# Kernel optimization log

Hardware: AMD Instinct MI355X
Metric: run time of the kernel (lower is better)

The kernel has to match this reference:

```python
import jax, jax.numpy as jnp
import numpy as np

B, H = 8192, 768


def _mk_linear(key, fan_in, fan_out):
    k1, k2 = jax.random.split(key)
    lim = 1.0 / np.sqrt(fan_in)
    W = jax.random.uniform(k1, (fan_out, fan_in), jnp.float32, -lim, lim)
    b = jax.random.uniform(k2, (fan_out,), jnp.float32, -lim, lim)
    return W, b


def setup_inputs() -> dict:
    key = jax.random.key(0)
    ks = jax.random.split(key, 6)
    modal_a = jax.random.normal(ks[0], (B, H), jnp.float32)
    modal_b = jax.random.normal(ks[1], (B, H), jnp.float32)
    W1m, b1m = _mk_linear(ks[2], H, H)
    W2m, b2m = _mk_linear(ks[3], H, H)
    W1v, b1v = _mk_linear(ks[4], H, H)
    W2v, b2v = _mk_linear(ks[5], H, H)
    return {"modal_a": modal_a, "modal_b": modal_b,
            "W1m": W1m, "b1m": b1m, "W2m": W2m, "b2m": b2m,
            "W1v": W1v, "b1v": b1v, "W2v": W2v, "b2v": b2v}


def reference(modal_a, modal_b, W1m, b1m, W2m, b2m, W1v, b1v, W2v, b2v):
    # mlp_mu: Linear -> Tanh -> Linear
    mu = jnp.tanh(modal_a @ W1m.T + b1m) @ W2m.T + b2m              # [B,H]
    # mlp_logvar: Linear -> Tanh -> Linear -> Tanh
    logvar = jnp.tanh(jnp.tanh(modal_a @ W1v.T + b1v) @ W2v.T + b2v)  # [B,H]
    inv_var = jnp.exp(-logvar)

    positive = -(mu - modal_b) ** 2 * 0.5 * inv_var                  # [B,H]

    # mean_j (mu[j] - mu[i])^2 = E[mu^2] - 2*mu[i]*E[mu] + mu[i]^2  (per feature dim)
    # Algebraic reduction of the O(B^2*H) tile in the original code.
    mu_mean = jnp.mean(mu, axis=0)                                   # [H]
    mu_sq_mean = jnp.mean(mu * mu, axis=0)                           # [H]
    pair_sq = mu_sq_mean - 2.0 * mu * mu_mean + mu * mu              # [B,H]
    negative = -pair_sq * 0.5 * inv_var                              # [B,H]

    pos_sum = jnp.sum(positive, axis=-1)                             # [B]
    neg_sum = jnp.sum(negative, axis=-1)                             # [B]
    lld = jnp.mean(pos_sum)
    bound = jnp.mean(pos_sum - neg_sum)
    return (lld, bound)
```

## Files before the change

kernel.cpp:

```cpp
#include <hip/hip_runtime.h>
#include <math.h>

typedef float v4f __attribute__((ext_vector_type(4)));
typedef short bf16x8 __attribute__((ext_vector_type(8)));

#define AS1 __attribute__((address_space(1)))
#define AS3 __attribute__((address_space(3)))

static constexpr int Bn = 8192;
static constexpr int Hn = 768;
static constexpr float invB = 1.0f / 8192.0f;

__device__ __forceinline__ short f32_to_bf16(float x) {
    union { float f; unsigned u; } v; v.f = x;
    unsigned r = (v.u + 0x7FFFu + ((v.u >> 16) & 1u)) >> 16;
    return (short)r;
}

__device__ __forceinline__ float fast_tanh(float x) {
    float xc = fminf(fmaxf(x, -15.0f), 15.0f);
    float e = __expf(2.0f * xc);
    float r = __builtin_amdgcn_rcpf(e + 1.0f);
    return 1.0f - 2.0f * r;
}

__global__ void prep_kernel(const float* __restrict__ A,
                            const float* __restrict__ W1m, const float* __restrict__ W2m,
                            const float* __restrict__ W1v, const float* __restrict__ W2v,
                            short* __restrict__ A_bf,
                            short* __restrict__ W1m_bf, short* __restrict__ W2m_bf,
                            short* __restrict__ W1v_bf, short* __restrict__ W2v_bf,
                            float* __restrict__ zbuf, int nzero) {
    const int tid = blockIdx.x * blockDim.x + threadIdx.x;
    if (tid < nzero) zbuf[tid] = 0.0f;
    constexpr int A4 = Bn * Hn / 4;
    constexpr int W4 = Hn * Hn / 4;
    const int total = A4 + 4 * W4;
    const int stride = gridDim.x * blockDim.x;
    for (int i = tid; i < total; i += stride) {
        const float* s; short* d; int j;
        if (i < A4) { s = A; d = A_bf; j = i; }
        else {
            int k = i - A4; int w = k / W4; j = k - w * W4;
            s = (w == 0) ? W1m : (w == 1) ? W2m : (w == 2) ? W1v : W2v;
            d = (w == 0) ? W1m_bf : (w == 1) ? W2m_bf : (w == 2) ? W1v_bf : W2v_bf;
        }
        float4 v = ((const float4*)s)[j];
        short4 o;
        o.x = f32_to_bf16(v.x); o.y = f32_to_bf16(v.y);
        o.z = f32_to_bf16(v.z); o.w = f32_to_bf16(v.w);
        ((short4*)d)[j] = o;
    }
}

__launch_bounds__(256, 3)
__global__ void gemm_l1(const short* __restrict__ A_g,
                        const short* __restrict__ Wm_g, const short* __restrict__ Wv_g,
                        const float* __restrict__ bm, const float* __restrict__ bv,
                        short* __restrict__ outm, short* __restrict__ outv) {
    constexpr int K = Hn;
    __shared__ __align__(16) short smem[16384];
    short* As = smem;
    short* Ws = smem + 8192;

    const int z = blockIdx.z;
    const short* W = z ? Wv_g : Wm_g;
    const float* bias = z ? bv : bm;
    short* out = z ? outv : outm;

    const int t = threadIdx.x;
    const int row0 = blockIdx.x * 128;
    const int col0 = blockIdx.y * 128;
    const int w = t >> 6, lane = t & 63;
    const int wm = w >> 1, wn = w & 1;
    const int lr = lane & 15, quad = lane >> 4;

    const int rt = t >> 3;
    const int bsrc = (t & 7) ^ (rt & 7);

    const short* pA[4]; const short* pW[4];
#pragma unroll
    for (int i = 0; i < 4; ++i) {
        pA[i] = A_g + (size_t)(row0 + i * 32 + rt) * K + bsrc * 8;
        pW[i] = W + (size_t)(col0 + i * 32 + rt) * K + bsrc * 8;
    }

    v4f acc[4][4] = {};

    for (int k0 = 0; k0 < K; k0 += 64) {
#pragma unroll
        for (int i = 0; i < 4; ++i) {
            __builtin_amdgcn_global_load_lds((AS1 void*)pA[i], (AS3 void*)&As[i * 2048 + t * 8], 16, 0, 0);
            __builtin_amdgcn_global_load_lds((AS1 void*)pW[i], (AS3 void*)&Ws[i * 2048 + t * 8], 16, 0, 0);
            pA[i] += 64; pW[i] += 64;
        }
        __syncthreads();
#pragma unroll
        for (int s = 0; s < 2; ++s) {
            const int kb = s * 4 + quad;
            bf16x8 af[4], bfr[4];
#pragma unroll
            for (int mt = 0; mt < 4; ++mt) {
                int m = wm * 64 + mt * 16 + lr;
                af[mt] = *(const bf16x8*)&As[m * 64 + ((kb ^ (m & 7)) << 3)];
            }
#pragma unroll
            for (int nt = 0; nt < 4; ++nt) {
                int n = wn * 64 + nt * 16 + lr;
                bfr[nt] = *(const bf16x8*)&Ws[n * 64 + ((kb ^ (n & 7)) << 3)];
            }
#pragma unroll
            for (int mt = 0; mt < 4; ++mt)
#pragma unroll
                for (int nt = 0; nt < 4; ++nt)
                    acc[mt][nt] = __builtin_amdgcn_mfma_f32_16x16x32_bf16(af[mt], bfr[nt], acc[mt][nt], 0, 0, 0);
        }
        __syncthreads();
    }

#pragma unroll
    for (int nt = 0; nt < 4; ++nt) {
        const int col_l = wn * 64 + nt * 16 + lr;
        const float bc = bias[col0 + col_l];
#pragma unroll
        for (int mt = 0; mt < 4; ++mt) {
#pragma unroll
            for (int r = 0; r < 4; ++r) {
                const int row_l = wm * 64 + mt * 16 + quad * 4 + r;
                smem[row_l * 128 + col_l] = f32_to_bf16(fast_tanh(acc[mt][nt][r] + bc));
            }
        }
    }
    __syncthreads();
#pragma unroll
    for (int p = 0; p < 8; ++p) {
        const int row_l = p * 16 + (t >> 4);
        const int seg = (t & 15) * 8;
        bf16x8 v = *(const bf16x8*)&smem[row_l * 128 + seg];
        *(bf16x8*)&out[(size_t)(row0 + row_l) * Hn + col0 + seg] = v;
    }
}

__launch_bounds__(256, 3)
__global__ void gemm_l2(const short* __restrict__ Am_g, const short* __restrict__ Av_g,
                        const short* __restrict__ Wm_g, const short* __restrict__ Wv_g,
                        const float* __restrict__ bm, const float* __restrict__ bv,
                        const float* __restrict__ mb,
                        float* __restrict__ cs, float* __restrict__ cs2,
                        float* __restrict__ siv, float* __restrict__ sivmu,
                        float* __restrict__ accum, float* __restrict__ outp) {
    constexpr int K = Hn;
    __shared__ __align__(16) short As_m[128 * 64];
    __shared__ __align__(16) short As_v[128 * 64];
    __shared__ __align__(16) short Ws_m[64 * 64];
    __shared__ __align__(16) short Ws_v[64 * 64];

    const int t = threadIdx.x;
    const int row0 = blockIdx.x * 128;
    const int col0 = blockIdx.y * 64;
    const int w = t >> 6, lane = t & 63;
    const int wm = w >> 1, wn = w & 1;
    const int lr = lane & 15, quad = lane >> 4;

    const int rt = t >> 3;
    const int bsrc = (t & 7) ^ (rt & 7);

    const short* pAm[4]; const short* pAv[4]; const short* pWm[2]; const short* pWv[2];
#pragma unroll
    for (int i = 0; i < 4; ++i) {
        pAm[i] = Am_g + (size_t)(row0 + i * 32 + rt) * K + bsrc * 8;
        pAv[i] = Av_g + (size_t)(row0 + i * 32 + rt) * K + bsrc * 8;
    }
#pragma unroll
    for (int i = 0; i < 2; ++i) {
        pWm[i] = Wm_g + (size_t)(col0 + i * 32 + rt) * K + bsrc * 8;
        pWv[i] = Wv_g + (size_t)(col0 + i * 32 + rt) * K + bsrc * 8;
    }

    v4f accm[4][2] = {}, accv[4][2] = {};

    for (int k0 = 0; k0 < K; k0 += 64) {
#pragma unroll
        for (int i = 0; i < 4; ++i) {
            __builtin_amdgcn_global_load_lds((AS1 void*)pAm[i], (AS3 void*)&As_m[i * 2048 + t * 8], 16, 0, 0);
            __builtin_amdgcn_global_load_lds((AS1 void*)pAv[i], (AS3 void*)&As_v[i * 2048 + t * 8], 16, 0, 0);
            pAm[i] += 64; pAv[i] += 64;
        }
#pragma unroll
        for (int i = 0; i < 2; ++i) {
            __builtin_amdgcn_global_load_lds((AS1 void*)pWm[i], (AS3 void*)&Ws_m[i * 2048 + t * 8], 16, 0, 0);
            __builtin_amdgcn_global_load_lds((AS1 void*)pWv[i], (AS3 void*)&Ws_v[i * 2048 + t * 8], 16, 0, 0);
            pWm[i] += 64; pWv[i] += 64;
        }
        __syncthreads();
#pragma unroll
        for (int s = 0; s < 2; ++s) {
            const int kb = s * 4 + quad;
            bf16x8 am[4], av[4], bmf[2], bvf[2];
#pragma unroll
            for (int mt = 0; mt < 4; ++mt) {
                int m = wm * 64 + mt * 16 + lr;
                int off = m * 64 + ((kb ^ (m & 7)) << 3);
                am[mt] = *(const bf16x8*)&As_m[off];
                av[mt] = *(const bf16x8*)&As_v[off];
            }
#pragma unroll
            for (int nt = 0; nt < 2; ++nt) {
                int n = wn * 32 + nt * 16 + lr;
                int off = n * 64 + ((kb ^ (n & 7)) << 3);
                bmf[nt] = *(const bf16x8*)&Ws_m[off];
                bvf[nt] = *(const bf16x8*)&Ws_v[off];
            }
#pragma unroll
            for (int mt = 0; mt < 4; ++mt)
#pragma unroll
                for (int nt = 0; nt < 2; ++nt) {
                    accm[mt][nt] = __builtin_amdgcn_mfma_f32_16x16x32_bf16(am[mt], bmf[nt], accm[mt][nt], 0, 0, 0);
                    accv[mt][nt] = __builtin_amdgcn_mfma_f32_16x16x32_bf16(av[mt], bvf[nt], accv[mt][nt], 0, 0, 0);
                }
        }
        __syncthreads();
    }

    float pos = 0.f, q = 0.f;
#pragma unroll
    for (int nt = 0; nt < 2; ++nt) {
        const int col = col0 + wn * 32 + nt * 16 + lr;
        const float bmc = bm[col], bvc = bv[col];
        float c1 = 0.f, c2 = 0.f, c3 = 0.f, c4 = 0.f;
#pragma unroll
        for (int mt = 0; mt < 4; ++mt) {
#pragma unroll
            for (int r = 0; r < 4; ++r) {
                const int row = row0 + wm * 64 + mt * 16 + quad * 4 + r;
                float mu = accm[mt][nt][r] + bmc;
                float tv = fast_tanh(accv[mt][nt][r] + bvc);
                float iv = __expf(-tv);
                float mbv = mb[(size_t)row * Hn + col];
                float d = mu - mbv;
                pos += iv * d * d;
                q   += iv * mu * mu;
                c1 += mu; c2 += mu * mu; c3 += iv; c4 += iv * mu;
            }
        }
        c1 += __shfl_xor(c1, 16); c1 += __shfl_xor(c1, 32);
        c2 += __shfl_xor(c2, 16); c2 += __shfl_xor(c2, 32);
        c3 += __shfl_xor(c3, 16); c3 += __shfl_xor(c3, 32);
        c4 += __shfl_xor(c4, 16); c4 += __shfl_xor(c4, 32);
        if (quad == 0) {
            atomicAdd(&cs[col], c1);
            atomicAdd(&cs2[col], c2);
            atomicAdd(&siv[col], c3);
            atomicAdd(&sivmu[col], c4);
        }
    }
    for (int off = 32; off > 0; off >>= 1) {
        pos += __shfl_down(pos, off);
        q   += __shfl_down(q, off);
    }
    __shared__ float redP[4], redQ[4];
    if (lane == 0) { redP[w] = pos; redQ[w] = q; }
    __syncthreads();
    __shared__ int is_last;
    if (t == 0) {
        atomicAdd(&accum[0], redP[0] + redP[1] + redP[2] + redP[3]);
        atomicAdd(&accum[1], redQ[0] + redQ[1] + redQ[2] + redQ[3]);
        __threadfence();
        unsigned old = atomicAdd((unsigned int*)&accum[3], 1u);
        is_last = (old == gridDim.x * gridDim.y - 1) ? 1 : 0;
    }
    __syncthreads();
    if (is_last) {
        float term = 0.f;
        for (int h = t; h < Hn; h += 256) {
            float v1 = atomicAdd(&cs[h], 0.0f);
            float v2 = atomicAdd(&cs2[h], 0.0f);
            float v3 = atomicAdd(&siv[h], 0.0f);
            float v4 = atomicAdd(&sivmu[h], 0.0f);
            term += v3 * v2 - 2.0f * v4 * v1;
        }
        for (int off = 32; off > 0; off >>= 1) term += __shfl_down(term, off);
        __shared__ float redT[4];
        if (lane == 0) redT[w] = term;
        __syncthreads();
        if (t == 0) {
            float T = redT[0] + redT[1] + redT[2] + redT[3];
            float P = atomicAdd(&accum[0], 0.0f);
            float Q = atomicAdd(&accum[1], 0.0f);
            float pos_sum = -0.5f * P;
            float neg_sum = -0.5f * (T * invB + Q);
            outp[0] = pos_sum * invB;
            outp[1] = (pos_sum - neg_sum) * invB;
        }
    }
}

extern "C" void kernel_launch(void* const* d_in, const int* in_sizes, int n_in,
                              void* d_out, int out_size, void* d_ws, size_t ws_size,
                              hipStream_t stream) {
    const float* modal_a = (const float*)d_in[0];
    const float* modal_b = (const float*)d_in[1];
    const float* W1m = (const float*)d_in[2];
    const float* b1m = (const float*)d_in[3];
    const float* W2m = (const float*)d_in[4];
    const float* b2m = (const float*)d_in[5];
    const float* W1v = (const float*)d_in[6];
    const float* b1v = (const float*)d_in[7];
    const float* W2v = (const float*)d_in[8];
    const float* b2v = (const float*)d_in[9];
    float* out = (float*)d_out;

    char* ws = (char*)d_ws;
    constexpr size_t szAH = (size_t)Bn * Hn * 2;
    constexpr size_t szW  = (size_t)Hn * Hn * 2;
    short* A_bf   = (short*)(ws);
    short* h1m    = (short*)(ws + szAH);
    short* h1v    = (short*)(ws + 2 * szAH);
    short* W1m_bf = (short*)(ws + 3 * szAH);
    short* W2m_bf = (short*)(ws + 3 * szAH + szW);
    short* W1v_bf = (short*)(ws + 3 * szAH + 2 * szW);
    short* W2v_bf = (short*)(ws + 3 * szAH + 3 * szW);
    float* cs     = (float*)(ws + 3 * szAH + 4 * szW);
    float* cs2    = cs + Hn;
    float* siv    = cs + 2 * Hn;
    float* sivmu  = cs + 3 * Hn;
    float* accum  = cs + 4 * Hn;

    prep_kernel<<<1280, 256, 0, stream>>>(modal_a, W1m, W2m, W1v, W2v,
                                          A_bf, W1m_bf, W2m_bf, W1v_bf, W2v_bf,
                                          cs, 4 * Hn + 8);

    gemm_l1<<<dim3(Bn / 128, Hn / 128, 2), 256, 0, stream>>>(
        A_bf, W1m_bf, W1v_bf, b1m, b1v, h1m, h1v);

    gemm_l2<<<dim3(Bn / 128, Hn / 64), 256, 0, stream>>>(
        h1m, h1v, W2m_bf, W2v_bf, b2m, b2v, modal_b,
        cs, cs2, siv, sivmu, accum, out);
}
```

Baseline: 181.9 us.

## Share A tile across mu/logvar GEMMs and widen layer-2 tile to 128 columns

```diff
diff --git a/kernel.cpp b/kernel.cpp
--- a/kernel.cpp
+++ b/kernel.cpp
@@ -53,20 +53,16 @@
     }
 }
 
-__launch_bounds__(256, 3)
+__launch_bounds__(256, 2)
 __global__ void gemm_l1(const short* __restrict__ A_g,
                         const short* __restrict__ Wm_g, const short* __restrict__ Wv_g,
                         const float* __restrict__ bm, const float* __restrict__ bv,
                         short* __restrict__ outm, short* __restrict__ outv) {
     constexpr int K = Hn;
-    __shared__ __align__(16) short smem[16384];
+    __shared__ __align__(16) short smem[24576];
     short* As = smem;
-    short* Ws = smem + 8192;
-
-    const int z = blockIdx.z;
-    const short* W = z ? Wv_g : Wm_g;
-    const float* bias = z ? bv : bm;
-    short* out = z ? outv : outm;
+    short* Wms = smem + 8192;
+    short* Wvs = smem + 16384;
 
     const int t = threadIdx.x;
     const int row0 = blockIdx.x * 128;
@@ -78,27 +74,29 @@
     const int rt = t >> 3;
     const int bsrc = (t & 7) ^ (rt & 7);
 
-    const short* pA[4]; const short* pW[4];
+    const short* pA[4]; const short* pWm[4]; const short* pWv[4];
 #pragma unroll
     for (int i = 0; i < 4; ++i) {
-        pA[i] = A_g + (size_t)(row0 + i * 32 + rt) * K + bsrc * 8;
-        pW[i] = W + (size_t)(col0 + i * 32 + rt) * K + bsrc * 8;
-    }
-
-    v4f acc[4][4] = {};
+        pA[i]  = A_g  + (size_t)(row0 + i * 32 + rt) * K + bsrc * 8;
+        pWm[i] = Wm_g + (size_t)(col0 + i * 32 + rt) * K + bsrc * 8;
+        pWv[i] = Wv_g + (size_t)(col0 + i * 32 + rt) * K + bsrc * 8;
+    }
+
+    v4f accm[4][4] = {}, accv[4][4] = {};
 
     for (int k0 = 0; k0 < K; k0 += 64) {
 #pragma unroll
         for (int i = 0; i < 4; ++i) {
-            __builtin_amdgcn_global_load_lds((AS1 void*)pA[i], (AS3 void*)&As[i * 2048 + t * 8], 16, 0, 0);
-            __builtin_amdgcn_global_load_lds((AS1 void*)pW[i], (AS3 void*)&Ws[i * 2048 + t * 8], 16, 0, 0);
-            pA[i] += 64; pW[i] += 64;
+            __builtin_amdgcn_global_load_lds((AS1 void*)pA[i],  (AS3 void*)&As[i * 2048 + t * 8], 16, 0, 0);
+            __builtin_amdgcn_global_load_lds((AS1 void*)pWm[i], (AS3 void*)&Wms[i * 2048 + t * 8], 16, 0, 0);
+            __builtin_amdgcn_global_load_lds((AS1 void*)pWv[i], (AS3 void*)&Wvs[i * 2048 + t * 8], 16, 0, 0);
+            pA[i] += 64; pWm[i] += 64; pWv[i] += 64;
         }
         __syncthreads();
 #pragma unroll
         for (int s = 0; s < 2; ++s) {
             const int kb = s * 4 + quad;
-            bf16x8 af[4], bfr[4];
+            bf16x8 af[4], fm[4], fv[4];
 #pragma unroll
             for (int mt = 0; mt < 4; ++mt) {
                 int m = wm * 64 + mt * 16 + lr;
@@ -107,41 +105,52 @@
 #pragma unroll
             for (int nt = 0; nt < 4; ++nt) {
                 int n = wn * 64 + nt * 16 + lr;
-                bfr[nt] = *(const bf16x8*)&Ws[n * 64 + ((kb ^ (n & 7)) << 3)];
+                int off = n * 64 + ((kb ^ (n & 7)) << 3);
+                fm[nt] = *(const bf16x8*)&Wms[off];
+                fv[nt] = *(const bf16x8*)&Wvs[off];
             }
 #pragma unroll
             for (int mt = 0; mt < 4; ++mt)
 #pragma unroll
-                for (int nt = 0; nt < 4; ++nt)
-                    acc[mt][nt] = __builtin_amdgcn_mfma_f32_16x16x32_bf16(af[mt], bfr[nt], acc[mt][nt], 0, 0, 0);
-        }
-        __syncthreads();
-    }
-
-#pragma unroll
-    for (int nt = 0; nt < 4; ++nt) {
-        const int col_l = wn * 64 + nt * 16 + lr;
-        const float bc = bias[col0 + col_l];
-#pragma unroll
-        for (int mt = 0; mt < 4; ++mt) {
-#pragma unroll
-            for (int r = 0; r < 4; ++r) {
-                const int row_l = wm * 64 + mt * 16 + quad * 4 + r;
-                smem[row_l * 128 + col_l] = f32_to_bf16(fast_tanh(acc[mt][nt][r] + bc));
-            }
-        }
-    }
-    __syncthreads();
-#pragma unroll
-    for (int p = 0; p < 8; ++p) {
-        const int row_l = p * 16 + (t >> 4);
-        const int seg = (t & 15) * 8;
-        bf16x8 v = *(const bf16x8*)&smem[row_l * 128 + seg];
-        *(bf16x8*)&out[(size_t)(row0 + row_l) * Hn + col0 + seg] = v;
-    }
-}
-
-__launch_bounds__(256, 3)
+                for (int nt = 0; nt < 4; ++nt) {
+                    accm[mt][nt] = __builtin_amdgcn_mfma_f32_16x16x32_bf16(af[mt], fm[nt], accm[mt][nt], 0, 0, 0);
+                    accv[mt][nt] = __builtin_amdgcn_mfma_f32_16x16x32_bf16(af[mt], fv[nt], accv[mt][nt], 0, 0, 0);
+                }
+        }
+        __syncthreads();
+    }
+
+#pragma unroll
+    for (int br = 0; br < 2; ++br) {
+        const float* bias = br ? bv : bm;
+        short* out = br ? outv : outm;
+#pragma unroll
+        for (int nt = 0; nt < 4; ++nt) {
+            const int col_l = wn * 64 + nt * 16 + lr;
+            const float bc = bias[col0 + col_l];
+#pragma unroll
+            for (int mt = 0; mt < 4; ++mt) {
+#pragma unroll
+                for (int r = 0; r < 4; ++r) {
+                    const int row_l = wm * 64 + mt * 16 + quad * 4 + r;
+                    float v = (br ? accv[mt][nt][r] : accm[mt][nt][r]) + bc;
+                    smem[row_l * 136 + col_l] = f32_to_bf16(fast_tanh(v));
+                }
+            }
+        }
+        __syncthreads();
+#pragma unroll
+        for (int p = 0; p < 8; ++p) {
+            const int c = p * 256 + t;
+            const int row = c >> 4, rem = c & 15;
+            bf16x8 v = *(const bf16x8*)&smem[row * 136 + rem * 8];
+            *(bf16x8*)&out[(size_t)(row0 + row) * Hn + col0 + rem * 8] = v;
+        }
+        __syncthreads();
+    }
+}
+
+__launch_bounds__(256, 2)
 __global__ void gemm_l2(const short* __restrict__ Am_g, const short* __restrict__ Av_g,
                         const short* __restrict__ Wm_g, const short* __restrict__ Wv_g,
                         const float* __restrict__ bm, const float* __restrict__ bv,
@@ -150,14 +159,15 @@
                         float* __restrict__ siv, float* __restrict__ sivmu,
                         float* __restrict__ accum, float* __restrict__ outp) {
     constexpr int K = Hn;
-    __shared__ __align__(16) short As_m[128 * 64];
-    __shared__ __align__(16) short As_v[128 * 64];
-    __shared__ __align__(16) short Ws_m[64 * 64];
-    __shared__ __align__(16) short Ws_v[64 * 64];
+    __shared__ __align__(16) short smem[32768];
+    short* Ams = smem;
+    short* Avs = smem + 8192;
+    short* Wms = smem + 16384;
+    short* Wvs = smem + 24576;
 
     const int t = threadIdx.x;
     const int row0 = blockIdx.x * 128;
-    const int col0 = blockIdx.y * 64;
+    const int col0 = blockIdx.y * 128;
     const int w = t >> 6, lane = t & 63;
     const int wm = w >> 1, wn = w & 1;
     const int lr = lane & 15, quad = lane >> 4;
@@ -165,58 +175,51 @@
     const int rt = t >> 3;
     const int bsrc = (t & 7) ^ (rt & 7);
 
-    const short* pAm[4]; const short* pAv[4]; const short* pWm[2]; const short* pWv[2];
+    const short* pAm[4]; const short* pAv[4]; const short* pWm[4]; const short* pWv[4];
 #pragma unroll
     for (int i = 0; i < 4; ++i) {
         pAm[i] = Am_g + (size_t)(row0 + i * 32 + rt) * K + bsrc * 8;
         pAv[i] = Av_g + (size_t)(row0 + i * 32 + rt) * K + bsrc * 8;
-    }
-#pragma unroll
-    for (int i = 0; i < 2; ++i) {
         pWm[i] = Wm_g + (size_t)(col0 + i * 32 + rt) * K + bsrc * 8;
         pWv[i] = Wv_g + (size_t)(col0 + i * 32 + rt) * K + bsrc * 8;
     }
 
-    v4f accm[4][2] = {}, accv[4][2] = {};
+    v4f accm[4][4] = {}, accv[4][4] = {};
 
     for (int k0 = 0; k0 < K; k0 += 64) {
 #pragma unroll
         for (int i = 0; i < 4; ++i) {
-            __builtin_amdgcn_global_load_lds((AS1 void*)pAm[i], (AS3 void*)&As_m[i * 2048 + t * 8], 16, 0, 0);
-            __builtin_amdgcn_global_load_lds((AS1 void*)pAv[i], (AS3 void*)&As_v[i * 2048 + t * 8], 16, 0, 0);
-            pAm[i] += 64; pAv[i] += 64;
-        }
-#pragma unroll
-        for (int i = 0; i < 2; ++i) {
-            __builtin_amdgcn_global_load_lds((AS1 void*)pWm[i], (AS3 void*)&Ws_m[i * 2048 + t * 8], 16, 0, 0);
-            __builtin_amdgcn_global_load_lds((AS1 void*)pWv[i], (AS3 void*)&Ws_v[i * 2048 + t * 8], 16, 0, 0);
-            pWm[i] += 64; pWv[i] += 64;
+            __builtin_amdgcn_global_load_lds((AS1 void*)pAm[i], (AS3 void*)&Ams[i * 2048 + t * 8], 16, 0, 0);
+            __builtin_amdgcn_global_load_lds((AS1 void*)pAv[i], (AS3 void*)&Avs[i * 2048 + t * 8], 16, 0, 0);
+            __builtin_amdgcn_global_load_lds((AS1 void*)pWm[i], (AS3 void*)&Wms[i * 2048 + t * 8], 16, 0, 0);
+            __builtin_amdgcn_global_load_lds((AS1 void*)pWv[i], (AS3 void*)&Wvs[i * 2048 + t * 8], 16, 0, 0);
+            pAm[i] += 64; pAv[i] += 64; pWm[i] += 64; pWv[i] += 64;
         }
         __syncthreads();
 #pragma unroll
         for (int s = 0; s < 2; ++s) {
             const int kb = s * 4 + quad;
-            bf16x8 am[4], av[4], bmf[2], bvf[2];
+            bf16x8 fam[4], fav[4], fwm[4], fwv[4];
 #pragma unroll
             for (int mt = 0; mt < 4; ++mt) {
                 int m = wm * 64 + mt * 16 + lr;
                 int off = m * 64 + ((kb ^ (m & 7)) << 3);
-                am[mt] = *(const bf16x8*)&As_m[off];
-                av[mt] = *(const bf16x8*)&As_v[off];
-            }
-#pragma unroll
-            for (int nt = 0; nt < 2; ++nt) {
-                int n = wn * 32 + nt * 16 + lr;
+                fam[mt] = *(const bf16x8*)&Ams[off];
+                fav[mt] = *(const bf16x8*)&Avs[off];
+            }
+#pragma unroll
+            for (int nt = 0; nt < 4; ++nt) {
+                int n = wn * 64 + nt * 16 + lr;
                 int off = n * 64 + ((kb ^ (n & 7)) << 3);
-                bmf[nt] = *(const bf16x8*)&Ws_m[off];
-                bvf[nt] = *(const bf16x8*)&Ws_v[off];
+                fwm[nt] = *(const bf16x8*)&Wms[off];
+                fwv[nt] = *(const bf16x8*)&Wvs[off];
             }
 #pragma unroll
             for (int mt = 0; mt < 4; ++mt)
 #pragma unroll
-                for (int nt = 0; nt < 2; ++nt) {
-                    accm[mt][nt] = __builtin_amdgcn_mfma_f32_16x16x32_bf16(am[mt], bmf[nt], accm[mt][nt], 0, 0, 0);
-                    accv[mt][nt] = __builtin_amdgcn_mfma_f32_16x16x32_bf16(av[mt], bvf[nt], accv[mt][nt], 0, 0, 0);
+                for (int nt = 0; nt < 4; ++nt) {
+                    accm[mt][nt] = __builtin_amdgcn_mfma_f32_16x16x32_bf16(fam[mt], fwm[nt], accm[mt][nt], 0, 0, 0);
+                    accv[mt][nt] = __builtin_amdgcn_mfma_f32_16x16x32_bf16(fav[mt], fwv[nt], accv[mt][nt], 0, 0, 0);
                 }
         }
         __syncthreads();
@@ -224,8 +227,8 @@
 
     float pos = 0.f, q = 0.f;
 #pragma unroll
-    for (int nt = 0; nt < 2; ++nt) {
-        const int col = col0 + wn * 32 + nt * 16 + lr;
+    for (int nt = 0; nt < 4; ++nt) {
+        const int col = col0 + wn * 64 + nt * 16 + lr;
         const float bmc = bm[col], bvc = bv[col];
         float c1 = 0.f, c2 = 0.f, c3 = 0.f, c4 = 0.f;
 #pragma unroll
@@ -330,10 +333,10 @@
                                           A_bf, W1m_bf, W2m_bf, W1v_bf, W2v_bf,
                                           cs, 4 * Hn + 8);
 
-    gemm_l1<<<dim3(Bn / 128, Hn / 128, 2), 256, 0, stream>>>(
+    gemm_l1<<<dim3(Bn / 128, Hn / 128), 256, 0, stream>>>(
         A_bf, W1m_bf, W1v_bf, b1m, b1v, h1m, h1v);
 
-    gemm_l2<<<dim3(Bn / 128, Hn / 64), 256, 0, stream>>>(
+    gemm_l2<<<dim3(Bn / 128, Hn / 128), 256, 0, stream>>>(
         h1m, h1v, W2m_bf, W2v_bf, b2m, b2v, modal_b,
         cs, cs2, siv, sivmu, accum, out);
 }
```

Result: no change. 184.2 us (+1.3%).
